# Kernel tuning notes

Hardware: AMD Instinct MI355X
Metric: run time of the kernel (lower is better)

The kernel has to match this reference:

```python
import jax, jax.numpy as jnp
import numpy as np

BATCH, T, N_STATE, N_CTRL = 16, 512, 64, 32


def setup_inputs() -> dict:
    key = jax.random.key(0)
    ks = jax.random.split(key, 6)
    n, m = N_STATE, N_CTRL
    # SPD per-step cost: Q = M M^T/(n+m) + I  (guarantees Q_uu invertible)
    M = jax.random.normal(ks[0], (BATCH, T, n + m, n + m), jnp.float32)
    Q = jnp.einsum('btij,btkj->btik', M, M) / (n + m) + jnp.eye(n + m, dtype=jnp.float32)
    p = jax.random.normal(ks[1], (BATCH, T, n + m), jnp.float32)
    # near-stable dynamics so the T-step rollout stays bounded
    A = 0.9 * jnp.eye(n, dtype=jnp.float32) + 0.02 * jax.random.normal(ks[2], (BATCH, T, n, n), jnp.float32)
    B = 0.1 * jax.random.normal(ks[3], (BATCH, T, n, m), jnp.float32)
    c1 = 0.1 * jax.random.normal(ks[4], (BATCH, T, n), jnp.float32)
    x_init = jax.random.normal(ks[5], (BATCH, n), jnp.float32)
    return {'Q': Q, 'p': p, 'A': A, 'B': B, 'c1': c1, 'x_init': x_init}


def _lqr(Q, p, A, B, c1, x_init):
    n = A.shape[-1]
    F = jnp.concatenate([A, B], axis=-1)                      # [b,T,n,n+m]
    # time-major for scan
    Qs = jnp.moveaxis(Q, 1, 0)
    ps = jnp.moveaxis(p, 1, 0)
    Fs = jnp.moveaxis(F, 1, 0)
    cs = jnp.moveaxis(c1, 1, 0)
    bsz = x_init.shape[0]
    V0 = jnp.zeros((bsz, n, n), Q.dtype)
    v0 = jnp.zeros((bsz, n), Q.dtype)

    def bstep(carry, inp):
        V, v = carry
        Qt, pt, Ft, ct = inp
        FtV = jnp.einsum('bij,bik->bjk', Ft, V)               # F^T V : [b,n+m,n]
        Qh = Qt + FtV @ Ft                                     # Q_t + F^T V F
        qh = pt + jnp.einsum('bij,bi->bj', Ft,
                             jnp.einsum('bij,bj->bi', V, ct) + v)
        Quu, Qux = Qh[:, n:, n:], Qh[:, n:, :n]
        Qxx, Qxu = Qh[:, :n, :n], Qh[:, :n, n:]
        qx, qu = qh[:, :n], qh[:, n:]
        L = jnp.linalg.cholesky(Quu)
        rhs = jnp.concatenate([Qux, qu[..., None]], axis=-1)   # solve K and k together
        sol = -jax.scipy.linalg.cho_solve((L, True), rhs)
        K, k = sol[..., :n], sol[..., n]
        QuuK = Quu @ K
        Vn = Qxx + Qxu @ K + jnp.einsum('bji,bjk->bik', K, Qux + QuuK)
        Vn = 0.5 * (Vn + jnp.swapaxes(Vn, -1, -2))             # keep symmetric
        vn = qx + jnp.einsum('bij,bj->bi', Qxu, k) \
             + jnp.einsum('bji,bj->bi', K, qu + jnp.einsum('bij,bj->bi', Quu, k))
        return (Vn, vn), (K, k)

    _, (Ks, ks) = jax.lax.scan(bstep, (V0, v0), (Qs, ps, Fs, cs), reverse=True)

    def fstep(x, inp):
        Kt, kt, At, Bt, ct = inp
        u = jnp.einsum('bij,bj->bi', Kt, x) + kt
        xn = jnp.einsum('bij,bj->bi', At, x) + jnp.einsum('bij,bj->bi', Bt, u) + ct
        return xn, (x, u)

    _, (xs, us) = jax.lax.scan(fstep, x_init,
                               (Ks, ks, jnp.moveaxis(A, 1, 0), jnp.moveaxis(B, 1, 0), cs))
    tau = jnp.concatenate([xs, us], axis=-1)                   # [T,b,n+m]
    return jnp.moveaxis(tau, 0, 1)                             # [b,T,n+m]


def reference(Q, p, A, B, c1, x_init):
    return _lqr(Q, p, A, B, c1, x_init)
```

## Files before the change

kernel.cpp:

```cpp
#include <hip/hip_runtime.h>
#include <math.h>

#define TT 512
#define NB 16

#define QH_B   0
#define LI_B   38400
#define T1_B   43008
#define VBH_B  52368
#define VBL_B  61584
#define FTH_B  70800
#define FTL_B  84624
#define WTH_B  98448
#define WTL_B  112272
#define XUH_B  126096
#define XUL_B  131216
#define KTH_B  136336
#define KTL_B  141456
#define QHF_B  146576
#define VV_B   146960
#define CV_B   147216
#define KV_B   147472
#define SMB    147600

#define AB0 0
#define AB1 6400
#define KF0 12800
#define KF1 14976
#define XB0 17152
#define XB1 17216
#define UBO 17280
#define AXO 17312

#define WSK_STRIDE 2080

typedef __attribute__((ext_vector_type(8))) short s8v;
typedef __attribute__((ext_vector_type(4))) float f4v;

__device__ __forceinline__ float lanebc(float x, int lane) {
    return __int_as_float(__builtin_amdgcn_readlane(__float_as_int(x), lane));
}
__device__ __forceinline__ float dot4(float4 a, float4 b) {
    return a.x * b.x + a.y * b.y + a.z * b.z + a.w * b.w;
}
__device__ __forceinline__ unsigned short f2bf(float x) {
    unsigned int u = __float_as_uint(x);
    u += 0x7FFFu + ((u >> 16) & 1u);
    return (unsigned short)(u >> 16);
}
__device__ __forceinline__ float bf2f(unsigned short h) {
    return __uint_as_float(((unsigned int)h) << 16);
}
__device__ __forceinline__ void pack4(const f4v d, ushort4* hp, ushort4* lp) {
    unsigned short h0 = f2bf(d[0]), h1 = f2bf(d[1]), h2 = f2bf(d[2]), h3 = f2bf(d[3]);
    *hp = make_ushort4(h0, h1, h2, h3);
    *lp = make_ushort4(f2bf(d[0] - bf2f(h0)), f2bf(d[1] - bf2f(h1)),
                       f2bf(d[2] - bf2f(h2)), f2bf(d[3] - bf2f(h3)));
}
__device__ __forceinline__ void tileMN(int T, int& mt, int& nt) {
    mt = (T >= 15) ? 5 : (T >= 10) ? 4 : (T >= 6) ? 3 : (T >= 3) ? 2 : (T >= 1) ? 1 : 0;
    nt = T - mt * (mt + 1) / 2;
}
#define MFMA(a,b,c) __builtin_amdgcn_mfma_f32_16x16x32_bf16((a),(b),(c),0,0,0)

__launch_bounds__(512, 2)
__global__ void lqr_kernel(const float* __restrict__ Q, const float* __restrict__ P,
                           const float* __restrict__ A, const float* __restrict__ B,
                           const float* __restrict__ c1, const float* __restrict__ xinit,
                           float* __restrict__ out, float* __restrict__ ws)
{
    __shared__ __align__(16) unsigned char smb[SMB];
    float*          QHf = (float*)(smb + QH_B);
    float*          LIf = (float*)(smb + LI_B);
    float*          T1f = (float*)(smb + T1_B);
    unsigned short* VBH = (unsigned short*)(smb + VBH_B);
    unsigned short* VBL = (unsigned short*)(smb + VBL_B);
    unsigned short* FTH = (unsigned short*)(smb + FTH_B);
    unsigned short* FTL = (unsigned short*)(smb + FTL_B);
    unsigned short* WTH = (unsigned short*)(smb + WTH_B);
    unsigned short* WTL = (unsigned short*)(smb + WTL_B);
    unsigned short* XUH = (unsigned short*)(smb + XUH_B);
    unsigned short* XUL = (unsigned short*)(smb + XUL_B);
    unsigned short* KTH = (unsigned short*)(smb + KTH_B);
    unsigned short* KTL = (unsigned short*)(smb + KTL_B);
    float*          QHF = (float*)(smb + QHF_B);
    float*          VVf = (float*)(smb + VV_B);
    float*          CVf = (float*)(smb + CV_B);
    float*          KVf = (float*)(smb + KV_B);

    const int tid = threadIdx.x;
    const int b   = blockIdx.x;
    const int wv  = tid >> 6;
    const int ln  = tid & 63;
    const int l15 = ln & 15;
    const int lq  = ln >> 4;
    float* wsK = ws;

    const int qcnt = (wv < 5) ? 3 : 2;
    const int qr = ln >> 2, qc4 = ln & 3;

    float4 qreg[3];
    {
        const float* Qg = Q + ((size_t)b * TT + (TT - 1)) * 9216;
#pragma unroll
        for (int tt = 0; tt < 3; ++tt) if (tt < qcnt) {
            int T = wv + 8 * tt, mt, nt; tileMN(T, mt, nt);
            qreg[tt] = *(const float4*)&Qg[(16 * mt + qr) * 96 + 16 * nt + 4 * qc4];
        }
    }

    if (tid < 384) {
        const size_t bt = (size_t)b * TT + (TT - 1);
        const int rb = tid & 15, cb = tid >> 4;
        float4 fr[4];
#pragma unroll
        for (int r = 0; r < 4; ++r) {
            const float* src = (cb < 16) ? (A + (bt * 64 + 4 * rb + r) * 64 + 4 * cb)
                                         : (B + (bt * 64 + 4 * rb + r) * 32 + 4 * (cb - 16));
            fr[r] = *(const float4*)src;
        }
#pragma unroll
        for (int c2 = 0; c2 < 4; ++c2) {
            f4v col;
            col[0] = ((const float*)&fr[0])[c2]; col[1] = ((const float*)&fr[1])[c2];
            col[2] = ((const float*)&fr[2])[c2]; col[3] = ((const float*)&fr[3])[c2];
            ushort4 hv, lv; pack4(col, &hv, &lv);
            *(ushort4*)&FTH[(4 * cb + c2) * 72 + 4 * rb] = hv;
            *(ushort4*)&FTL[(4 * cb + c2) * 72 + 4 * rb] = lv;
        }
    } else {
        float* vb = (float*)VBH;
        for (int i = tid - 384; i < 4608; i += 128) vb[i] = 0.0f;
        if (tid >= 448) VVf[tid - 448] = 0.0f;
    }
    __syncthreads();

    for (int t = TT - 1; t >= 0; --t) {
        const size_t bt  = (size_t)b * TT + t;
        const size_t btp = (size_t)b * TT + ((t > 0) ? (t - 1) : 0);

#pragma unroll
        for (int tt = 0; tt < 3; ++tt) if (tt < qcnt) {
            int T = wv + 8 * tt, mt, nt; tileMN(T, mt, nt);
            *(float4*)&QHf[(16 * mt + qr) * 100 + 16 * nt + 4 * qc4] = qreg[tt];
        }
        {
            const float* Qg = Q + btp * 9216;
#pragma unroll
            for (int tt = 0; tt < 3; ++tt) if (tt < qcnt) {
                int T = wv + 8 * tt, mt, nt; tileMN(T, mt, nt);
                qreg[tt] = *(const float4*)&Qg[(16 * mt + qr) * 96 + 16 * nt + 4 * qc4];
            }
        }
        float4 fp4[4];
        if (wv >= 1 && wv <= 6) {
            const int tau = tid - 64, rb = tau & 15, cb = tau >> 4;
#pragma unroll
            for (int r = 0; r < 4; ++r) {
                const float* src = (cb < 16) ? (A + (btp * 64 + 4 * rb + r) * 64 + 4 * cb)
                                             : (B + (btp * 64 + 4 * rb + r) * 32 + 4 * (cb - 16));
                fp4[r] = *(const float4*)src;
            }
        }
        if (wv == 7 && ln < 16)
            *(float4*)&CVf[4 * ln] = *(const float4*)&c1[bt * 64 + 4 * ln];
        float pv = 0.0f;
        if (ln < 48 && (ln & 3) == 0) pv = P[bt * 96 + 12 * wv + (ln >> 2)];

        auto g1Tile = [&](int mt, int nt) {
            const unsigned short* ah = VBH + (16 * nt + l15) * 72 + 8 * lq;
            const unsigned short* al = VBL + (16 * nt + l15) * 72 + 8 * lq;
            const unsigned short* bh = FTH + (16 * mt + l15) * 72 + 8 * lq;
            const unsigned short* bl = FTL + (16 * mt + l15) * 72 + 8 * lq;
            f4v d = {0.0f, 0.0f, 0.0f, 0.0f};
#pragma unroll
            for (int kc = 0; kc < 2; ++kc) {
                s8v Ah = *(const s8v*)(ah + 32 * kc);
                s8v Al = *(const s8v*)(al + 32 * kc);
                s8v Bh = *(const s8v*)(bh + 32 * kc);
                s8v Bl = *(const s8v*)(bl + 32 * kc);
                d = MFMA(Ah, Bh, d);
                d = MFMA(Ah, Bl, d);
                d = MFMA(Al, Bh, d);
            }
            int wi = 16 * nt + 4 * lq, wc = 16 * mt + l15;
            ushort4 hv, lv; pack4(d, &hv, &lv);
            *(ushort4*)&WTH[wc * 72 + wi] = hv;
            *(ushort4*)&WTL[wc * 72 + wi] = lv;
        };
        auto qhTile = [&](int T) {
            int mt, nt; tileMN(T, mt, nt);
            int orow = 16 * mt + 4 * lq, ocol = 16 * nt + l15;
            const unsigned short* ah = FTH + (16 * mt + l15) * 72 + 8 * lq;
            const unsigned short* al = FTL + (16 * mt + l15) * 72 + 8 * lq;
            const unsigned short* bh = WTH + (16 * nt + l15) * 72 + 8 * lq;
            const unsigned short* bl = WTL + (16 * nt + l15) * 72 + 8 * lq;
            f4v d;
#pragma unroll
            for (int rr = 0; rr < 4; ++rr)
                d[rr] = QHf[(orow + rr) * 100 + ocol];
#pragma unroll
            for (int kc = 0; kc < 2; ++kc) {
                s8v Ah = *(const s8v*)(ah + 32 * kc);
                s8v Al = *(const s8v*)(al + 32 * kc);
                s8v Bh = *(const s8v*)(bh + 32 * kc);
                s8v Bl = *(const s8v*)(bl + 32 * kc);
                d = MFMA(Ah, Bh, d);
                d = MFMA(Ah, Bl, d);
                d = MFMA(Al, Bh, d);
            }
#pragma unroll
            for (int rr = 0; rr < 4; ++rr)
                QHf[(orow + rr) * 100 + ocol] = d[rr];
            if (mt > nt) {
#pragma unroll
                for (int rr = 0; rr < 4; ++rr)
                    QHf[ocol * 100 + orow + rr] = d[rr];
            }
            if (mt >= 4 && nt < 4) {
                ushort4 hx, lx; pack4(d, &hx, &lx);
                *(ushort4*)&XUH[ocol * 40 + (orow - 64)] = hx;
                *(ushort4*)&XUL[ocol * 40 + (orow - 64)] = lx;
            }
        };

        {
            g1Tile(4 + (wv >> 2), wv & 3);
            if (ln < 48) {
                int row = 12 * wv + (ln >> 2), kq = ln & 3;
                float acc = 0.0f;
                const unsigned short* fh = FTH + row * 72 + 16 * kq;
                const unsigned short* fl = FTL + row * 72 + 16 * kq;
                const float* vvp = VVf + 16 * kq;
#pragma unroll
                for (int k = 0; k < 16; ++k)
                    acc += (bf2f(fh[k]) + bf2f(fl[k])) * vvp[k];
                acc += __shfl_xor(acc, 1);
                acc += __shfl_xor(acc, 2);
                if ((ln & 3) == 0) QHF[row] = acc + pv;
            }
        }
        __syncthreads();

        if (wv == 0) {
            qhTile(14); qhTile(19); qhTile(20);
        } else {
            int g0 = wv - 1;  g1Tile(g0 >> 2, g0 & 3);
            int g1 = 6 + wv;  g1Tile(g1 >> 2, g1 & 3);
            if (wv <= 2) { int g2 = 13 + wv; g1Tile(g2 >> 2, g2 & 3); }
        }
        __syncthreads();

        if (wv == 0) {
            __builtin_amdgcn_s_setprio(1);
            const int i = ln & 31;
            float a[32];
#pragma unroll
            for (int j4 = 0; j4 < 8; ++j4) {
                float4 v = *(const float4*)&QHf[(64 + i) * 100 + 64 + 4 * j4];
                a[4 * j4] = v.x; a[4 * j4 + 1] = v.y; a[4 * j4 + 2] = v.z; a[4 * j4 + 3] = v.w;
            }
#pragma unroll
            for (int j = 0; j < 32; ++j) {
                float dj = lanebc(a[j], j);
                float rj = rsqrtf(dj);
                a[j] *= rj;
#pragma unroll
                for (int k = j + 1; k < 32; ++k)
                    a[k] -= a[j] * lanebc(a[j], k);
            }
            float y[32];
#pragma unroll
            for (int r = 0; r < 32; ++r) {
                float acc0 = (r == i) ? 1.0f : 0.0f, acc1 = 0.0f;
#pragma unroll
                for (int j = 0; j < r; ++j) {
                    float lrj = lanebc(a[j], r);
                    if (j & 1) acc1 -= lrj * y[j]; else acc0 -= lrj * y[j];
                }
                y[r] = (acc0 + acc1) * __builtin_amdgcn_rcpf(lanebc(a[r], r));
            }
            __builtin_amdgcn_s_setprio(0);
            if (ln < 32) {
#pragma unroll
                for (int r = 0; r < 32; ++r) LIf[r * 36 + ln] = y[r];
            }
        } else if (wv == 7) {
#pragma unroll
            for (int pass = 0; pass < 2; ++pass) {
                int j = pass ? (64 + (ln & 31)) : ln;
                if (pass && ln >= 32) break;
                float acc = QHF[j];
                const unsigned short* wh = WTH + j * 72;
                const unsigned short* wl = WTL + j * 72;
#pragma unroll 4
                for (int i = 0; i < 64; ++i)
                    acc += (bf2f(wh[i]) + bf2f(wl[i])) * CVf[i];
                QHf[j * 100 + 96] = acc;
            }
        } else {
            int ta, tb, tc;
            switch (wv) {
                case 1: ta = 10; tb = 15; tc = 0; break;
                case 2: ta = 11; tb = 16; tc = 1; break;
                case 3: ta = 12; tb = 17; tc = 2; break;
                case 4: ta = 13; tb = 18; tc = 3; break;
                case 5: ta = 4;  tb = 5;  tc = 6; break;
                default: ta = 7; tb = 8;  tc = 9; break;
            }
            qhTile(ta); qhTile(tb); qhTile(tc);
        }
        __syncthreads();

        {
            const int c = tid & 63, rq = tid >> 6;
            f4v acc = {0.0f, 0.0f, 0.0f, 0.0f};
#pragma unroll
            for (int j4 = 0; j4 < 8; ++j4) {
                float4 qv = *(const float4*)&QHf[c * 100 + 64 + 4 * j4];
#pragma unroll
                for (int rr = 0; rr < 4; ++rr) {
                    float4 li = *(const float4*)&LIf[(4 * rq + rr) * 36 + 4 * j4];
                    acc[rr] += dot4(li, qv);
                }
            }
            *(f4v*)&T1f[c * 36 + 4 * rq] = acc;
            if (tid < 32) {
                float aq = 0.0f;
#pragma unroll 4
                for (int j = 0; j < 32; ++j)
                    aq += LIf[tid * 36 + j] * QHf[(64 + j) * 100 + 96];
                T1f[64 * 36 + tid] = aq;
            }
            if (wv >= 1 && wv <= 6) {
                const int tau = tid - 64, rb = tau & 15, cb = tau >> 4;
#pragma unroll
                for (int c2 = 0; c2 < 4; ++c2) {
                    f4v col;
                    col[0] = ((const float*)&fp4[0])[c2]; col[1] = ((const float*)&fp4[1])[c2];
                    col[2] = ((const float*)&fp4[2])[c2]; col[3] = ((const float*)&fp4[3])[c2];
                    ushort4 hv, lv; pack4(col, &hv, &lv);
                    *(ushort4*)&FTH[(4 * cb + c2) * 72 + 4 * rb] = hv;
                    *(ushort4*)&FTL[(4 * cb + c2) * 72 + 4 * rb] = lv;
                }
            }
        }
        __syncthreads();

        {
            const int c = tid & 63, jq = tid >> 6;
            f4v acc = {0.0f, 0.0f, 0.0f, 0.0f};
#pragma unroll
            for (int i4 = 0; i4 < 8; ++i4) {
                float4 tv = *(const float4*)&T1f[c * 36 + 4 * i4];
#pragma unroll
                for (int ii = 0; ii < 4; ++ii) {
                    float4 li = *(const float4*)&LIf[(4 * i4 + ii) * 36 + 4 * jq];
                    float tvi = (ii == 0) ? tv.x : (ii == 1) ? tv.y : (ii == 2) ? tv.z : tv.w;
                    acc[0] += tvi * li.x; acc[1] += tvi * li.y;
                    acc[2] += tvi * li.z; acc[3] += tvi * li.w;
                }
            }
            f4v kv; kv[0] = -acc[0]; kv[1] = -acc[1]; kv[2] = -acc[2]; kv[3] = -acc[3];
            ushort4 hk, lk; pack4(kv, &hk, &lk);
            *(ushort4*)&KTH[c * 40 + 4 * jq] = hk;
            *(ushort4*)&KTL[c * 40 + 4 * jq] = lk;
            float* wrow = wsK + bt * WSK_STRIDE;
#pragma unroll
            for (int jj = 0; jj < 4; ++jj)
                wrow[(4 * jq + jj) * 65 + c] = kv[jj];
            if (tid < 32) {
                float aq = 0.0f;
#pragma unroll 4
                for (int i = 0; i < 32; ++i)
                    aq += LIf[i * 36 + tid] * T1f[64 * 36 + i];
                KVf[tid] = -aq;
                wsK[bt * WSK_STRIDE + tid * 65 + 64] = -aq;
            }
        }
        __syncthreads();

        {
#pragma unroll
            for (int tt = 0; tt < 2; ++tt) {
                int T = 2 * wv + tt, mt = T >> 2, nt = T & 3;
                f4v d;
#pragma unroll
                for (int rr = 0; rr < 4; ++rr)
                    d[rr] = QHf[(16 * nt + 4 * lq + rr) * 100 + 16 * mt + l15];
                s8v Ah = *(const s8v*)(KTH + (16 * nt + l15) * 40 + 8 * lq);
                s8v Al = *(const s8v*)(KTL + (16 * nt + l15) * 40 + 8 * lq);
                s8v Bh = *(const s8v*)(XUH + (16 * mt + l15) * 40 + 8 * lq);
                s8v Bl = *(const s8v*)(XUL + (16 * mt + l15) * 40 + 8 * lq);
                d = MFMA(Ah, Bh, d);
                d = MFMA(Ah, Bl, d);
                d = MFMA(Al, Bh, d);
                ushort4 hv, lv; pack4(d, &hv, &lv);
                *(ushort4*)&VBH[(16 * mt + l15) * 72 + 16 * nt + 4 * lq] = hv;
                *(ushort4*)&VBL[(16 * mt + l15) * 72 + 16 * nt + 4 * lq] = lv;
            }
            {
                int r = 8 * wv + (ln >> 3), kq = ln & 7;
                float acc = 0.0f;
#pragma unroll
                for (int e = 0; e < 4; ++e) {
                    int j = 4 * kq + e;
                    acc += QHf[r * 100 + 64 + j] * KVf[j];
                }
                acc += __shfl_xor(acc, 1);
                acc += __shfl_xor(acc, 2);
                acc += __shfl_xor(acc, 4);
                if (kq == 0) VVf[r] = acc + QHf[r * 100 + 96];
            }
        }
        __syncthreads();
    }

    float* sm = (float*)smb;
    {
        const size_t bt0 = (size_t)b * TT;
#pragma unroll
        for (int it = 0; it < 3; ++it) {
            int q = tid + 512 * it, row = q / 24, g = q % 24;
            const float* src = (g < 16) ? (A + (bt0 * 64 + row) * 64 + 4 * g)
                                        : (B + (bt0 * 64 + row) * 32 + 4 * (g - 16));
            *(float4*)&sm[AB0 + row * 100 + 4 * g] = *(const float4*)src;
        }
#pragma unroll
        for (int i = 0; i < 5; ++i) {
            int idx = tid + 512 * i;
            if (idx < 2080) {
                int j = idx / 65, c = idx - 65 * j;
                sm[KF0 + j * 68 + c] = wsK[bt0 * WSK_STRIDE + idx];
            }
        }
        if (tid < 64) sm[XB0 + tid] = xinit[b * 64 + tid];
    }
    __syncthreads();

    for (int t = 0; t < TT; ++t) {
        const size_t bt  = (size_t)b * TT + t;
        const size_t btn = (size_t)b * TT + ((t < TT - 1) ? (t + 1) : t);
        const int cur = t & 1;
        const int abC = cur ? AB1 : AB0, abN = cur ? AB0 : AB1;
        const int kfC = cur ? KF1 : KF0, kfN = cur ? KF0 : KF1;
        const int xbC = cur ? XB1 : XB0, xbN = cur ? XB0 : XB1;

        float4 abpre[6];
        float kpre[9];
        float cpre = 0.0f;
        if (tid >= 256) {
            const int t2 = tid - 256;
#pragma unroll
            for (int it = 0; it < 6; ++it) {
                int q = t2 + 256 * it, row = q / 24, g = q % 24;
                const float* src = (g < 16) ? (A + (btn * 64 + row) * 64 + 4 * g)
                                            : (B + (btn * 64 + row) * 32 + 4 * (g - 16));
                abpre[it] = *(const float4*)src;
            }
#pragma unroll
            for (int i = 0; i < 9; ++i) {
                int idx = t2 + 256 * i;
                kpre[i] = (idx < 2080) ? wsK[btn * WSK_STRIDE + idx] : 0.0f;
            }
            cpre = c1[bt * 64 + ((tid - 256) >> 2)];
        }

        if (tid < 256) {
            const int j = tid >> 3, q = tid & 7;
            float4 k0 = *(const float4*)&sm[kfC + j * 68 + 8 * q];
            float4 k1 = *(const float4*)&sm[kfC + j * 68 + 8 * q + 4];
            float4 x0 = *(const float4*)&sm[xbC + 8 * q];
            float4 x1 = *(const float4*)&sm[xbC + 8 * q + 4];
            float pa = dot4(k0, x0) + dot4(k1, x1);
            pa += __shfl_xor(pa, 1);
            pa += __shfl_xor(pa, 2);
            pa += __shfl_xor(pa, 4);
            if (q == 0) {
                float u = pa + sm[kfC + j * 68 + 64];
                sm[UBO + j] = u;
                out[bt * 96 + 64 + j] = u;
            }
        } else {
            const int r = (tid - 256) >> 2, q = tid & 3;
            float pa = 0.0f;
#pragma unroll
            for (int e4 = 0; e4 < 4; ++e4) {
                float4 av = *(const float4*)&sm[abC + r * 100 + 16 * q + 4 * e4];
                float4 xv = *(const float4*)&sm[xbC + 16 * q + 4 * e4];
                pa += dot4(av, xv);
            }
            pa += __shfl_xor(pa, 1);
            pa += __shfl_xor(pa, 2);
            if (q == 0) sm[AXO + r] = pa + cpre;
            if (q == 1) out[bt * 96 + r] = sm[xbC + r];
        }
        __syncthreads();

        if (tid < 256) {
            const int r = tid >> 2, q = tid & 3;
            float4 b0 = *(const float4*)&sm[abC + r * 100 + 64 + 8 * q];
            float4 b1 = *(const float4*)&sm[abC + r * 100 + 64 + 8 * q + 4];
            float4 u0 = *(const float4*)&sm[UBO + 8 * q];
            float4 u1 = *(const float4*)&sm[UBO + 8 * q + 4];
            float pa = dot4(b0, u0) + dot4(b1, u1);
            pa += __shfl_xor(pa, 1);
            pa += __shfl_xor(pa, 2);
            if (q == 0) sm[xbN + r] = sm[AXO + r] + pa;
        } else {
            const int t2 = tid - 256;
#pragma unroll
            for (int it = 0; it < 6; ++it) {
                int q = t2 + 256 * it, row = q / 24, g = q % 24;
                *(float4*)&sm[abN + row * 100 + 4 * g] = abpre[it];
            }
#pragma unroll
            for (int i = 0; i < 9; ++i) {
                int idx = t2 + 256 * i;
                if (idx < 2080) {
                    int j = idx / 65, c = idx - 65 * j;
                    sm[kfN + j * 68 + c] = kpre[i];
                }
            }
        }
        __syncthreads();
    }
}

extern "C" void kernel_launch(void* const* d_in, const int* in_sizes, int n_in,
                              void* d_out, int out_size, void* d_ws, size_t ws_size,
                              hipStream_t stream) {
    (void)in_sizes; (void)n_in; (void)out_size;
    const float* Q  = (const float*)d_in[0];
    const float* p  = (const float*)d_in[1];
    const float* A  = (const float*)d_in[2];
    const float* B  = (const float*)d_in[3];
    const float* c1 = (const float*)d_in[4];
    const float* xi = (const float*)d_in[5];
    if (ws_size < (size_t)NB * TT * WSK_STRIDE * sizeof(float)) return;
    lqr_kernel<<<NB, 512, 0, stream>>>(Q, p, A, B, c1, xi, (float*)d_out, (float*)d_ws);
}
```

Before: 8.756 ms.

## Rewrite value update as -T1ᵀT1 to drop K dependency and a barrier

The value-function update now uses T1 = L⁻¹Qux directly: Qxu·K becomes -T1ᵀT1 and Qxu·k becomes -T1ᵀ(L⁻¹qu). T1 is packed into positive and sign-flipped bf16 hi/lo buffers when it is computed, so the V-update MFMAs no longer wait for the gain K. That lets the V update share a stage with the K computation and removes one __syncthreads from each of the 512 sequential backward steps. The XU and KT staging buffers go away, and four extra bf16 stores are added per T1 element.

```diff
diff --git a/kernel.cpp b/kernel.cpp
--- a/kernel.cpp
+++ b/kernel.cpp
@@ -13,14 +13,13 @@
 #define FTL_B  84624
 #define WTH_B  98448
 #define WTL_B  112272
-#define XUH_B  126096
-#define XUL_B  131216
-#define KTH_B  136336
-#define KTL_B  141456
+#define T1PH_B 126096
+#define T1PL_B 131216
+#define T1MH_B 136336
+#define T1ML_B 141456
 #define QHF_B  146576
 #define VV_B   146960
 #define CV_B   147216
-#define KV_B   147472
 #define SMB    147600
 
 #define AB0 0
@@ -79,14 +78,13 @@
     unsigned short* FTL = (unsigned short*)(smb + FTL_B);
     unsigned short* WTH = (unsigned short*)(smb + WTH_B);
     unsigned short* WTL = (unsigned short*)(smb + WTL_B);
-    unsigned short* XUH = (unsigned short*)(smb + XUH_B);
-    unsigned short* XUL = (unsigned short*)(smb + XUL_B);
-    unsigned short* KTH = (unsigned short*)(smb + KTH_B);
-    unsigned short* KTL = (unsigned short*)(smb + KTL_B);
+    unsigned short* T1PH = (unsigned short*)(smb + T1PH_B);
+    unsigned short* T1PL = (unsigned short*)(smb + T1PL_B);
+    unsigned short* T1MH = (unsigned short*)(smb + T1MH_B);
+    unsigned short* T1ML = (unsigned short*)(smb + T1ML_B);
     float*          QHF = (float*)(smb + QHF_B);
     float*          VVf = (float*)(smb + VV_B);
     float*          CVf = (float*)(smb + CV_B);
-    float*          KVf = (float*)(smb + KV_B);
 
     const int tid = threadIdx.x;
     const int b   = blockIdx.x;
@@ -217,11 +215,6 @@
                 for (int rr = 0; rr < 4; ++rr)
                     QHf[ocol * 100 + orow + rr] = d[rr];
             }
-            if (mt >= 4 && nt < 4) {
-                ushort4 hx, lx; pack4(d, &hx, &lx);
-                *(ushort4*)&XUH[ocol * 40 + (orow - 64)] = hx;
-                *(ushort4*)&XUL[ocol * 40 + (orow - 64)] = lx;
-            }
         };
 
         {
@@ -325,6 +318,17 @@
                 }
             }
             *(f4v*)&T1f[c * 36 + 4 * rq] = acc;
+            {
+                ushort4 ph, pl; pack4(acc, &ph, &pl);
+                *(ushort4*)&T1PH[c * 40 + 4 * rq] = ph;
+                *(ushort4*)&T1PL[c * 40 + 4 * rq] = pl;
+                ushort4 mh = make_ushort4((unsigned short)(ph.x ^ 0x8000u), (unsigned short)(ph.y ^ 0x8000u),
+                                          (unsigned short)(ph.z ^ 0x8000u), (unsigned short)(ph.w ^ 0x8000u));
+                ushort4 ml = make_ushort4((unsigned short)(pl.x ^ 0x8000u), (unsigned short)(pl.y ^ 0x8000u),
+                                          (unsigned short)(pl.z ^ 0x8000u), (unsigned short)(pl.w ^ 0x8000u));
+                *(ushort4*)&T1MH[c * 40 + 4 * rq] = mh;
+                *(ushort4*)&T1ML[c * 40 + 4 * rq] = ml;
+            }
             if (tid < 32) {
                 float aq = 0.0f;
 #pragma unroll 4
@@ -361,26 +365,17 @@
                     acc[2] += tvi * li.z; acc[3] += tvi * li.w;
                 }
             }
-            f4v kv; kv[0] = -acc[0]; kv[1] = -acc[1]; kv[2] = -acc[2]; kv[3] = -acc[3];
-            ushort4 hk, lk; pack4(kv, &hk, &lk);
-            *(ushort4*)&KTH[c * 40 + 4 * jq] = hk;
-            *(ushort4*)&KTL[c * 40 + 4 * jq] = lk;
             float* wrow = wsK + bt * WSK_STRIDE;
 #pragma unroll
             for (int jj = 0; jj < 4; ++jj)
-                wrow[(4 * jq + jj) * 65 + c] = kv[jj];
+                wrow[(4 * jq + jj) * 65 + c] = -acc[jj];
             if (tid < 32) {
                 float aq = 0.0f;
 #pragma unroll 4
                 for (int i = 0; i < 32; ++i)
                     aq += LIf[i * 36 + tid] * T1f[64 * 36 + i];
-                KVf[tid] = -aq;
                 wsK[bt * WSK_STRIDE + tid * 65 + 64] = -aq;
             }
-        }
-        __syncthreads();
-
-        {
 #pragma unroll
             for (int tt = 0; tt < 2; ++tt) {
                 int T = 2 * wv + tt, mt = T >> 2, nt = T & 3;
@@ -388,10 +383,10 @@
 #pragma unroll
                 for (int rr = 0; rr < 4; ++rr)
                     d[rr] = QHf[(16 * nt + 4 * lq + rr) * 100 + 16 * mt + l15];
-                s8v Ah = *(const s8v*)(KTH + (16 * nt + l15) * 40 + 8 * lq);
-                s8v Al = *(const s8v*)(KTL + (16 * nt + l15) * 40 + 8 * lq);
-                s8v Bh = *(const s8v*)(XUH + (16 * mt + l15) * 40 + 8 * lq);
-                s8v Bl = *(const s8v*)(XUL + (16 * mt + l15) * 40 + 8 * lq);
+                s8v Ah = *(const s8v*)(T1MH + (16 * nt + l15) * 40 + 8 * lq);
+                s8v Al = *(const s8v*)(T1ML + (16 * nt + l15) * 40 + 8 * lq);
+                s8v Bh = *(const s8v*)(T1PH + (16 * mt + l15) * 40 + 8 * lq);
+                s8v Bl = *(const s8v*)(T1PL + (16 * mt + l15) * 40 + 8 * lq);
                 d = MFMA(Ah, Bh, d);
                 d = MFMA(Ah, Bl, d);
                 d = MFMA(Al, Bh, d);
@@ -401,16 +396,13 @@
             }
             {
                 int r = 8 * wv + (ln >> 3), kq = ln & 7;
-                float acc = 0.0f;
-#pragma unroll
-                for (int e = 0; e < 4; ++e) {
-                    int j = 4 * kq + e;
-                    acc += QHf[r * 100 + 64 + j] * KVf[j];
-                }
-                acc += __shfl_xor(acc, 1);
-                acc += __shfl_xor(acc, 2);
-                acc += __shfl_xor(acc, 4);
-                if (kq == 0) VVf[r] = acc + QHf[r * 100 + 96];
+                float4 t1r = *(const float4*)&T1f[r * 36 + 4 * kq];
+                float4 t1q = *(const float4*)&T1f[64 * 36 + 4 * kq];
+                float acc2 = dot4(t1r, t1q);
+                acc2 += __shfl_xor(acc2, 1);
+                acc2 += __shfl_xor(acc2, 2);
+                acc2 += __shfl_xor(acc2, 4);
+                if (kq == 0) VVf[r] = QHf[r * 100 + 96] - acc2;
             }
         }
         __syncthreads();
```

Result: faster. 8.355 ms (median of 3 runs) (-4.6%).
